# Optimization experiments

Hardware: AMD Instinct MI355X
Metric: run time of the kernel (lower is better)

## Reference

```python
import jax, jax.numpy as jnp
import numpy as np

N_NODES = 100000
N_EDGES = 1600000
N_REL = 8      # num_node_types in the torch module, used as relation count
D_IN = 128
D_HID = 128
D_OUT = 64


def setup_inputs() -> dict:
    key = jax.random.key(0)
    ks = jax.random.split(key, 16)
    x = jax.random.normal(ks[0], (N_NODES, D_IN), dtype=jnp.float32)
    edge_index = jax.random.randint(ks[1], (2, N_EDGES), 0, N_NODES, dtype=jnp.int64)
    edge_type = jax.random.randint(ks[2], (N_EDGES,), 0, N_REL, dtype=jnp.int64)
    # Glorot-ish init scale for stability
    def w(k, shape):
        fan = shape[-2] + shape[-1]
        return jax.random.normal(k, shape, dtype=jnp.float32) * jnp.sqrt(2.0 / fan)
    params = {
        'Wrel1': w(ks[3], (N_REL, D_IN, D_HID)),  'Wroot1': w(ks[4], (D_IN, D_HID)),  'b1': jnp.zeros((D_HID,), jnp.float32),
        'Wrel2': w(ks[5], (N_REL, D_HID, D_HID)), 'Wroot2': w(ks[6], (D_HID, D_HID)), 'b2': jnp.zeros((D_HID,), jnp.float32),
        'Wrel3': w(ks[7], (N_REL, D_HID, D_OUT)), 'Wroot3': w(ks[8], (D_HID, D_OUT)), 'b3': jnp.zeros((D_OUT,), jnp.float32),
    }
    return {'x': x, 'edge_index': edge_index, 'edge_type': edge_type, **params}


def _rgcn_conv(x, src, dst, edge_type, Wrel, Wroot, b):
    # Per-relation transform of all nodes: [R, N, out] (small GEMMs),
    # then per-edge gather + scatter-add (the memory-bound part).
    h = jnp.einsum('ni,rio->rno', x, Wrel)          # [R, N, out]
    msgs = h[edge_type, src]                        # [E, out] irregular gather
    agg = jax.ops.segment_sum(msgs, dst, num_segments=x.shape[0])  # [N, out]
    return x @ Wroot + b + agg


def reference(x, edge_index, edge_type, Wrel1, Wroot1, b1, Wrel2, Wroot2, b2, Wrel3, Wroot3, b3):
    src, dst = edge_index[0], edge_index[1]
    # Dropout is identity in eval mode (training=False in the torch module).
    h = jax.nn.relu(_rgcn_conv(x, src, dst, edge_type, Wrel1, Wroot1, b1))
    h = jax.nn.relu(_rgcn_conv(h, src, dst, edge_type, Wrel2, Wroot2, b2))
    h = _rgcn_conv(h, src, dst, edge_type, Wrel3, Wroot3, b3)
    return jax.nn.log_softmax(h, axis=-1)
```

## Files before the change

### kernel.cpp

```cpp
#include <hip/hip_runtime.h>


#define DEVI __device__ __forceinline__

typedef __attribute__((ext_vector_type(8))) short bf16x8;
typedef __attribute__((ext_vector_type(4))) float f32x4;

DEVI unsigned short f2b(float f) {
  unsigned int u = __builtin_bit_cast(unsigned int, f);
  unsigned int r = (u + 0x7FFFu + ((u >> 16) & 1u)) >> 16;
  return (unsigned short)r;
}
DEVI float b2f(unsigned short h) {
  unsigned int u = ((unsigned int)h) << 16;
  return __builtin_bit_cast(float, u);
}
DEVI float lo16f(unsigned v) { return __builtin_bit_cast(float, v << 16); }
DEVI float hifraw(unsigned v) { return __builtin_bit_cast(float, v); }
DEVI int imin(int a, int b) { return a < b ? a : b; }
DEVI int imax(int a, int b) { return a > b ? a : b; }


__global__ void k_zero2(int* __restrict__ cnt, int n) {
  int stride = gridDim.x * blockDim.x;
  for (int i = blockIdx.x * blockDim.x + threadIdx.x; i < n; i += stride) cnt[i] = 0;
}

__global__ void k_chist(const int* __restrict__ et, const int* __restrict__ edst,
                        int* __restrict__ gh, int NG, int E) {
  __shared__ int h[128];
  if (threadIdx.x < 128) h[threadIdx.x] = 0;
  __syncthreads();
  int stride = gridDim.x * blockDim.x;
  for (int i = blockIdx.x * blockDim.x + threadIdx.x; i < E; i += stride)
    atomicAdd(&h[(et[i] & 7) * NG + (edst[i] >> 13)], 1);
  __syncthreads();
  if (threadIdx.x < 128) atomicAdd(&gh[threadIdx.x], h[threadIdx.x]);
}

__global__ void k_cscan(const int* __restrict__ gh, int* __restrict__ gcursor,
                        int* __restrict__ cbase, int NBC, int E) {
  if (threadIdx.x == 0) {
    int a = 0;
    for (int b = 0; b < NBC; ++b) { cbase[b] = a; gcursor[b] = a; a += gh[b]; }
    cbase[NBC] = E;
  }
}

__launch_bounds__(256)
__global__ void k_cfill(const int* __restrict__ et, const int* __restrict__ esrc,
                        const int* __restrict__ edst, int* __restrict__ gcursor,
                        int* __restrict__ stage, int NG, int E) {
  __shared__ int h[128], base[128], lc[128];
  int nb = gridDim.x;
  int slice = (E + nb - 1) / nb;
  int lo = blockIdx.x * slice;
  int hi = lo + slice < E ? lo + slice : E;
  int t = threadIdx.x;
  if (t < 128) { h[t] = 0; lc[t] = 0; }
  __syncthreads();
  for (int i = lo + t; i < hi; i += 256)
    atomicAdd(&h[(et[i] & 7) * NG + (edst[i] >> 13)], 1);
  __syncthreads();
  if (t < 128 && h[t] > 0) base[t] = atomicAdd(&gcursor[t], h[t]);
  __syncthreads();
  for (int i = lo + t; i < hi; i += 256) {
    int d = edst[i];
    int tile = d >> 6;
    int bin = (et[i] & 7) * NG + (tile >> 7);
    int p = base[bin] + atomicAdd(&lc[bin], 1);
    stage[p] = ((tile & 127) << 23) | ((d & 63) << 17) | esrc[i];
  }
}

__launch_bounds__(1024)
__global__ void k_fine(const int* __restrict__ cbase, const int* __restrict__ stage,
                       int* __restrict__ srcl, int* __restrict__ lo9,
                       int* __restrict__ len9, int NG, int NTr) {
  __shared__ int h[8192];
  __shared__ int tsum[1024];
  __shared__ int wsum[16];
  int b = blockIdx.x;
  int rel = b / NG, tg = b - rel * NG;
  int lo = cbase[b], hi = cbase[b + 1];
  int t = threadIdx.x;
  for (int k = t; k < 8192; k += 1024) h[k] = 0;
  __syncthreads();
  for (int i = lo + t; i < hi; i += 1024)
    atomicAdd(&h[(stage[i] >> 17) & 0x1FFF], 1);
  __syncthreads();
  int dbase = tg * 8192;
  size_t relbase = (size_t)rel * NTr;
  for (int k = t; k < 8192; k += 1024) {
    int d = dbase + k;
    if (d < NTr) len9[relbase + d] = h[k];
  }
  int loc[8];
  int s = 0;
  int kb = t * 8;
#pragma unroll
  for (int j = 0; j < 8; ++j) { loc[j] = s; s += h[kb + j]; }
  tsum[t] = s;
  __syncthreads();
  int lane = t & 63, w = t >> 6;
  int v = tsum[t];
#pragma unroll
  for (int o = 1; o < 64; o <<= 1) {
    int u = __shfl_up(v, o);
    if (lane >= o) v += u;
  }
  if (lane == 63) wsum[w] = v;
  __syncthreads();
  if (t == 0) {
    int a = 0;
#pragma unroll
    for (int j = 0; j < 16; ++j) { int tmp = wsum[j]; wsum[j] = a; a += tmp; }
  }
  __syncthreads();
  int texcl = v - s + wsum[w];
#pragma unroll
  for (int j = 0; j < 8; ++j) h[kb + j] = texcl + loc[j];
  __syncthreads();
  for (int k = t; k < 8192; k += 1024) {
    int d = dbase + k;
    if (d < NTr) lo9[relbase + d] = lo + h[k];
  }
  __syncthreads();
  for (int i = lo + t; i < hi; i += 1024) {
    int pk = stage[i];
    int key = (pk >> 17) & 0x1FFF;
    int p = atomicAdd(&h[key], 1);
    srcl[lo + p] = pk & 0x1FFFF;
  }
}


__global__ void wprep_kernel(const float* __restrict__ Wrel, const float* __restrict__ Wroot,
                             unsigned short* __restrict__ wt, int DOUT) {
  int total = 9 * 128 * DOUT;
  int stride = gridDim.x * blockDim.x;
  for (int i = blockIdx.x * blockDim.x + threadIdx.x; i < total; i += stride) {
    int k = i & 127;
    int oo = i >> 7;
    int o = oo % DOUT;
    int rr = oo / DOUT;
    float v = (rr < 8) ? Wrel[((size_t)rr * 128 + k) * DOUT + o]
                       : Wroot[(size_t)k * DOUT + o];
    wt[i] = f2b(v);
  }
}


template <int NRP>
__launch_bounds__(256)
__global__ void agg_kernel(const unsigned* __restrict__ x32,
                           const int* __restrict__ lo9, const int* __restrict__ len9,
                           const int* __restrict__ srcl,
                           unsigned* __restrict__ Ydw,
                           int r0, int N, int E, int NTr) {
  int lane = threadIdx.x & 63;
  int d = (blockIdx.x * blockDim.x + threadIdx.x) >> 6;
  if (d >= N) return;

  int lo[NRP], ln[NRP];
#pragma unroll
  for (int r = 0; r < NRP; ++r) {
    size_t idx = (size_t)(r0 + r) * NTr + d;
    lo[r] = lo9[idx];
    ln[r] = len9[idx];
  }

  int s[NRP][4];
#pragma unroll
  for (int r = 0; r < NRP; ++r) {
    int lo_c = imin(lo[r], E - 1);
    int jmax = imax(ln[r] - 1, 0);
#pragma unroll
    for (int j = 0; j < 4; ++j)
      s[r][j] = srcl[lo_c + imin(j, jmax)];
  }

  unsigned v[NRP][4];
#pragma unroll
  for (int r = 0; r < NRP; ++r)
#pragma unroll
    for (int j = 0; j < 4; ++j)
      v[r][j] = x32[(size_t)s[r][j] * 64 + lane];

#pragma unroll
  for (int r = 0; r < NRP; ++r) {
    float a0 = 0.f, a1 = 0.f;
#pragma unroll
    for (int j = 0; j < 4; ++j) {
      if (ln[r] > j) { a0 += lo16f(v[r][j]); a1 += hifraw(v[r][j]); }
    }
    if (ln[r] > 4) {
      int i = lo[r] + 4, e = lo[r] + ln[r];
      for (; i + 2 <= e; i += 2) {
        int sA = srcl[i], sB = srcl[i + 1];
        unsigned vA = x32[(size_t)sA * 64 + lane];
        unsigned vB = x32[(size_t)sB * 64 + lane];
        a0 += lo16f(vA) + lo16f(vB);
        a1 += hifraw(vA) + hifraw(vB);
      }
      if (i < e) {
        unsigned vA = x32[(size_t)srcl[i] * 64 + lane];
        a0 += lo16f(vA);
        a1 += hifraw(vA);
      }
    }
    Ydw[(size_t)d * (NRP * 64) + r * 64 + lane] =
        (unsigned)f2b(a0) | ((unsigned)f2b(a1) << 16);
  }
}


struct SrcArr {
  const unsigned short* a[9];
  const unsigned short* w[9];
  int st[9];
};

template <int DOUT, int NK, int EPI>
__launch_bounds__(256)
__global__ void gemm_lds(SrcArr S, const float* __restrict__ bias,
                         const unsigned short* __restrict__ part,
                         unsigned short* __restrict__ out_b,
                         float* __restrict__ out_f, int N) {
  __shared__ unsigned short Al[2][64 * 128];
  constexpr int NF = (DOUT == 128) ? 2 : 1;
  int tid = threadIdx.x, wid = tid >> 6, lane = tid & 63;
  int colb = lane & 15, kgrp = lane >> 4;
  int colw = wid * 16 * NF;
  int tile = gridDim.x - 1 - blockIdx.x;
  int tilebase = tile * 64;

  auto stage = [&](int t, int buf) {
    const unsigned short* sa = S.a[t] + (size_t)tilebase * S.st[t];
    int st = S.st[t];
#pragma unroll
    for (int q = 0; q < 4; ++q) {
      int c = q * 256 + tid;
      int row = c >> 4, kcl = c & 15;
      int kcg = kcl ^ (row & 7);
      const unsigned short* gp = sa + (size_t)row * st + kcg * 8;
      unsigned short* lp = &Al[buf][(q * 256 + (tid & ~63)) * 8];
      __builtin_amdgcn_global_load_lds(
          (__attribute__((address_space(1))) void*)gp,
          (__attribute__((address_space(3))) void*)lp, 16, 0, 0);
    }
  };

  f32x4 acc[4][NF];
#pragma unroll
  for (int rb = 0; rb < 4; ++rb)
#pragma unroll
    for (int nf = 0; nf < NF; ++nf) {
      f32x4 z = {0.f, 0.f, 0.f, 0.f};
      acc[rb][nf] = z;
    }

  stage(0, 0);
#pragma unroll
  for (int t = 0; t < NK; ++t) {
    __syncthreads();
    if (t + 1 < NK) stage(t + 1, (t + 1) & 1);
    const unsigned short* W = S.w[t];
    const unsigned short* Ab = Al[t & 1];
#pragma unroll
    for (int kk = 0; kk < 4; ++kk) {
      int kc = kk * 4 + kgrp;
      bf16x8 a[4];
#pragma unroll
      for (int rb = 0; rb < 4; ++rb) {
        int arow = rb * 16 + colb;
        a[rb] = *(const bf16x8*)(Ab + (size_t)(arow * 16 + (kc ^ (arow & 7))) * 8);
      }
#pragma unroll
      for (int nf = 0; nf < NF; ++nf) {
        bf16x8 b = *(const bf16x8*)(W + (size_t)(colw + nf * 16 + colb) * 128 + kc * 8);
#pragma unroll
        for (int rb = 0; rb < 4; ++rb)
          acc[rb][nf] = __builtin_amdgcn_mfma_f32_16x16x32_bf16(a[rb], b, acc[rb][nf], 0, 0, 0);
      }
    }
  }

  float bv[NF];
  if (EPI == 0 || EPI == 3 || EPI == 4) {
#pragma unroll
    for (int nf = 0; nf < NF; ++nf) bv[nf] = bias[colw + nf * 16 + colb];
  }

  if ((EPI == 2 || EPI == 4) && DOUT == 64) {
    float* Lf = (float*)Al;
    __syncthreads();
#pragma unroll
    for (int rb = 0; rb < 4; ++rb)
#pragma unroll
      for (int i = 0; i < 4; ++i) {
        int row = rb * 16 + kgrp * 4 + i;
        int grow = tilebase + row;
        int rc = grow < N ? grow : 0;
        float v = acc[rb][0][i];
        if (EPI == 4) v += bv[0];
        else v += b2f(part[(size_t)rc * 64 + colw + colb]);
        Lf[row * 68 + colw + colb] = v;
      }
    __syncthreads();
#pragma unroll
    for (int it = 0; it < 4; ++it) {
      int row = wid * 16 + it * 4 + (lane >> 4);
      float v[4];
#pragma unroll
      for (int j = 0; j < 4; ++j) v[j] = Lf[row * 68 + colb + j * 16];
      float m = fmaxf(fmaxf(v[0], v[1]), fmaxf(v[2], v[3]));
#pragma unroll
      for (int s = 1; s < 16; s <<= 1) m = fmaxf(m, __shfl_xor(m, s));
      float sum = 0.f;
#pragma unroll
      for (int j = 0; j < 4; ++j) sum += __expf(v[j] - m);
#pragma unroll
      for (int s = 1; s < 16; s <<= 1) sum += __shfl_xor(sum, s);
      float lse = m + __logf(sum);
      int grow = tilebase + row;
      if (grow < N) {
#pragma unroll
        for (int j = 0; j < 4; ++j)
          out_f[(size_t)grow * 64 + colb + j * 16] = v[j] - lse;
      }
    }
  } else {
#pragma unroll
    for (int rb = 0; rb < 4; ++rb)
#pragma unroll
      for (int i = 0; i < 4; ++i) {
        int row = tilebase + rb * 16 + kgrp * 4 + i;
        bool ok = row < N;
        int rc = ok ? row : 0;
#pragma unroll
        for (int nf = 0; nf < NF; ++nf) {
          int col = colw + nf * 16 + colb;
          float v = acc[rb][nf][i];
          if (EPI == 0 || EPI == 3) v += bv[nf];
          if (EPI == 1 || EPI == 5) v += b2f(part[(size_t)rc * DOUT + col]);
          if (EPI == 1 || EPI == 3) v = fmaxf(v, 0.f);
          if (ok) out_b[(size_t)row * DOUT + col] = f2b(v);
        }
      }
  }
}

template <int DOUT>
static void run_gemm(int NK, int EPI, const SrcArr& S, const float* bias,
                     const unsigned short* part, unsigned short* ob, float* of,
                     int N, int NT, hipStream_t st) {
#define GCALL(nk, epi)                                                        \
  if (NK == nk && EPI == epi) {                                               \
    gemm_lds<DOUT, nk, epi><<<NT, 256, 0, st>>>(S, bias, part, ob, of, N);    \
    return;                                                                   \
  }
  GCALL(9, 3) GCALL(9, 4)
  GCALL(5, 0) GCALL(4, 1) GCALL(4, 2)
  GCALL(3, 0) GCALL(2, 5) GCALL(2, 1) GCALL(2, 2)
#undef GCALL
}


__global__ void cast_kernel(const float* __restrict__ in, unsigned short* __restrict__ out,
                            int n4) {
  int stride = gridDim.x * blockDim.x;
  for (int i = blockIdx.x * blockDim.x + threadIdx.x; i < n4; i += stride) {
    float4 v = ((const float4*)in)[i];
    ushort4 o;
    o.x = f2b(v.x); o.y = f2b(v.y); o.z = f2b(v.z); o.w = f2b(v.w);
    ((ushort4*)out)[i] = o;
  }
}


extern "C" void kernel_launch(void* const* d_in, const int* in_sizes, int n_in,
                              void* d_out, int out_size, void* d_ws, size_t ws_size,
                              hipStream_t stream) {
  const float* x = (const float*)d_in[0];
  const int* eidx = (const int*)d_in[1];
  const int* et = (const int*)d_in[2];
  const float* Wrel1 = (const float*)d_in[3];
  const float* Wroot1 = (const float*)d_in[4];
  const float* b1 = (const float*)d_in[5];
  const float* Wrel2 = (const float*)d_in[6];
  const float* Wroot2 = (const float*)d_in[7];
  const float* b2 = (const float*)d_in[8];
  const float* Wrel3 = (const float*)d_in[9];
  const float* Wroot3 = (const float*)d_in[10];
  const float* b3 = (const float*)d_in[11];

  const int N = in_sizes[0] / 128;
  const int E = in_sizes[2];
  const int NT = (N + 63) / 64;
  const int NTr = NT * 64;
  const int NG = (NT + 127) / 128;
  const int NBC = 8 * NG;
  const int* esrc = eidx;
  const int* edst = eidx + E;

  const size_t XB = (size_t)NTr * 128 * 2;

  size_t fixedB = XB + 2 * ((size_t)9 * 128 * 128 * 2) + (size_t)9 * 64 * 128 * 2 +
                  2 * ((size_t)E * 4) + 2 * ((size_t)8 * NTr * 4) + 8192;
  int NRP = 8;
  if (fixedB + 8 * XB > ws_size) NRP = 4;
  if (NRP == 4 && fixedB + XB + 4 * XB > ws_size) NRP = 2;

  char* p = (char*)d_ws;
  auto carve = [&](size_t bytes) {
    void* q = (void*)p;
    p += (bytes + 255) & ~(size_t)255;
    return q;
  };
  unsigned short* bufX = (unsigned short*)carve(XB);
  unsigned short* wt1 = (unsigned short*)carve((size_t)9 * 128 * 128 * 2);
  unsigned short* wt2 = (unsigned short*)carve((size_t)9 * 128 * 128 * 2);
  unsigned short* wt3 = (unsigned short*)carve((size_t)9 * 64 * 128 * 2);
  int* stage = (int*)carve((size_t)E * 4);
  int* srcl = (int*)carve((size_t)E * 4);
  int* lo9 = (int*)carve((size_t)8 * NTr * 4);
  int* len9 = (int*)carve((size_t)8 * NTr * 4);
  int* gh = (int*)carve(512);
  int* gcursor = (int*)carve(512);
  int* cbase = (int*)carve(512);
  unsigned short* part = (unsigned short*)((NRP < 8) ? carve(XB) : nullptr);
  unsigned short* Y = (unsigned short*)carve((size_t)NRP * XB);

  k_zero2<<<1, 128, 0, stream>>>(gh, 128);
  k_chist<<<512, 256, 0, stream>>>(et, edst, gh, NG, E);
  k_cscan<<<1, 64, 0, stream>>>(gh, gcursor, cbase, NBC, E);
  k_cfill<<<512, 256, 0, stream>>>(et, esrc, edst, gcursor, stage, NG, E);
  k_fine<<<NBC, 1024, 0, stream>>>(cbase, stage, srcl, lo9, len9, NG, NTr);

  wprep_kernel<<<576, 256, 0, stream>>>(Wrel1, Wroot1, wt1, 128);
  wprep_kernel<<<576, 256, 0, stream>>>(Wrel2, Wroot2, wt2, 128);
  wprep_kernel<<<288, 256, 0, stream>>>(Wrel3, Wroot3, wt3, 64);
  cast_kernel<<<2048, 256, 0, stream>>>(x, bufX, N * 128 / 4);

  const int ablk = (N * 64 + 255) / 256;
  const int passes = 8 / NRP;

  auto layer = [&](const unsigned short* xin, const unsigned short* wt,
                   const float* bias, int DOUT, unsigned short* xout, float* fout) {
    for (int pidx = 0; pidx < passes; ++pidx) {
      int r0 = pidx * NRP;
      if (NRP == 8)
        agg_kernel<8><<<ablk, 256, 0, stream>>>((const unsigned*)xin, lo9, len9, srcl, (unsigned*)Y, r0, N, E, NTr);
      else if (NRP == 4)
        agg_kernel<4><<<ablk, 256, 0, stream>>>((const unsigned*)xin, lo9, len9, srcl, (unsigned*)Y, r0, N, E, NTr);
      else
        agg_kernel<2><<<ablk, 256, 0, stream>>>((const unsigned*)xin, lo9, len9, srcl, (unsigned*)Y, r0, N, E, NTr);

      SrcArr S;
      int idx = 0;
      if (pidx == 0) {
        S.a[0] = xin; S.w[0] = wt + (size_t)8 * DOUT * 128; S.st[0] = 128;
        idx = 1;
      }
      for (int j = 0; j < NRP; ++j) {
        S.a[idx] = Y + j * 128;
        S.w[idx] = wt + (size_t)(r0 + j) * DOUT * 128;
        S.st[idx] = NRP * 128;
        ++idx;
      }
      int NK = idx;
      int epi;
      bool lastp = (pidx == passes - 1);
      if (pidx == 0 && lastp) epi = (DOUT == 64) ? 4 : 3;
      else if (pidx == 0) epi = 0;
      else if (!lastp) epi = 5;
      else epi = (DOUT == 64) ? 2 : 1;

      unsigned short* ob = lastp ? xout : part;
      if (pidx == 0 && !lastp) ob = part;
      if (DOUT == 128)
        run_gemm<128>(NK, epi, S, bias, part, ob, fout, N, NT, stream);
      else
        run_gemm<64>(NK, epi, S, bias, part, ob, fout, N, NT, stream);
    }
  };

  layer(bufX, wt1, b1, 128, bufX, nullptr);
  layer(bufX, wt2, b2, 128, bufX, nullptr);
  layer(bufX, wt3, b3, 64, nullptr, (float*)d_out);
}
```

Baseline: 638.3 us.

## Chunk layers over node tiles so aggregated buffer stays cache-resident

Restructures each layer to process node tiles in chunks: aggregation writes a per-chunk Y buffer that the fused 9-way GEMM immediately consumes, instead of materializing Y for all nodes. Uses ping-pong activation buffers since chunked processing can no longer update in place. Aims to keep the intermediate in L2/last-level cache and cut DRAM traffic, at the cost of more launches and smaller grids per launch.

```diff
diff --git a/kernel.cpp b/kernel.cpp
--- a/kernel.cpp
+++ b/kernel.cpp
@@ -19,6 +19,7 @@
 DEVI float hifraw(unsigned v) { return __builtin_bit_cast(float, v); }
 DEVI int imin(int a, int b) { return a < b ? a : b; }
 DEVI int imax(int a, int b) { return a > b ? a : b; }
+static inline int hmin(int a, int b) { return a < b ? a : b; }
 
 
 __global__ void k_zero2(int* __restrict__ cnt, int n) {
@@ -151,21 +152,22 @@
 }
 
 
-template <int NRP>
 __launch_bounds__(256)
 __global__ void agg_kernel(const unsigned* __restrict__ x32,
                            const int* __restrict__ lo9, const int* __restrict__ len9,
                            const int* __restrict__ srcl,
                            unsigned* __restrict__ Ydw,
-                           int r0, int N, int E, int NTr) {
+                           int N, int E, int NTr, int row0) {
+  constexpr int NRP = 8;
   int lane = threadIdx.x & 63;
-  int d = (blockIdx.x * blockDim.x + threadIdx.x) >> 6;
+  int dl = (blockIdx.x * blockDim.x + threadIdx.x) >> 6;
+  int d = row0 + dl;
   if (d >= N) return;
 
   int lo[NRP], ln[NRP];
 #pragma unroll
   for (int r = 0; r < NRP; ++r) {
-    size_t idx = (size_t)(r0 + r) * NTr + d;
+    size_t idx = (size_t)r * NTr + d;
     lo[r] = lo9[idx];
     ln[r] = len9[idx];
   }
@@ -209,7 +211,7 @@
         a1 += hifraw(vA);
       }
     }
-    Ydw[(size_t)d * (NRP * 64) + r * 64 + lane] =
+    Ydw[(size_t)dl * 512 + r * 64 + lane] =
         (unsigned)f2b(a0) | ((unsigned)f2b(a1) << 16);
   }
 }
@@ -219,24 +221,25 @@
   const unsigned short* a[9];
   const unsigned short* w[9];
   int st[9];
+  int ro[9];
 };
 
-template <int DOUT, int NK, int EPI>
+template <int DOUT, int EPI>
 __launch_bounds__(256)
 __global__ void gemm_lds(SrcArr S, const float* __restrict__ bias,
-                         const unsigned short* __restrict__ part,
                          unsigned short* __restrict__ out_b,
-                         float* __restrict__ out_f, int N) {
+                         float* __restrict__ out_f, int N, int c0) {
+  constexpr int NK = 9;
   __shared__ unsigned short Al[2][64 * 128];
   constexpr int NF = (DOUT == 128) ? 2 : 1;
   int tid = threadIdx.x, wid = tid >> 6, lane = tid & 63;
   int colb = lane & 15, kgrp = lane >> 4;
   int colw = wid * 16 * NF;
-  int tile = gridDim.x - 1 - blockIdx.x;
+  int tile = c0 + (gridDim.x - 1 - blockIdx.x);
   int tilebase = tile * 64;
 
   auto stage = [&](int t, int buf) {
-    const unsigned short* sa = S.a[t] + (size_t)tilebase * S.st[t];
+    const unsigned short* sa = S.a[t] + (size_t)(tilebase - S.ro[t]) * S.st[t];
     int st = S.st[t];
 #pragma unroll
     for (int q = 0; q < 4; ++q) {
@@ -287,12 +290,10 @@
   }
 
   float bv[NF];
-  if (EPI == 0 || EPI == 3 || EPI == 4) {
-#pragma unroll
-    for (int nf = 0; nf < NF; ++nf) bv[nf] = bias[colw + nf * 16 + colb];
-  }
-
-  if ((EPI == 2 || EPI == 4) && DOUT == 64) {
+#pragma unroll
+  for (int nf = 0; nf < NF; ++nf) bv[nf] = bias[colw + nf * 16 + colb];
+
+  if (EPI == 4 && DOUT == 64) {
     float* Lf = (float*)Al;
     __syncthreads();
 #pragma unroll
@@ -300,12 +301,7 @@
 #pragma unroll
       for (int i = 0; i < 4; ++i) {
         int row = rb * 16 + kgrp * 4 + i;
-        int grow = tilebase + row;
-        int rc = grow < N ? grow : 0;
-        float v = acc[rb][0][i];
-        if (EPI == 4) v += bv[0];
-        else v += b2f(part[(size_t)rc * 64 + colw + colb]);
-        Lf[row * 68 + colw + colb] = v;
+        Lf[row * 68 + colw + colb] = acc[rb][0][i] + bv[0];
       }
     __syncthreads();
 #pragma unroll
@@ -336,34 +332,15 @@
 #pragma unroll
       for (int i = 0; i < 4; ++i) {
         int row = tilebase + rb * 16 + kgrp * 4 + i;
-        bool ok = row < N;
-        int rc = ok ? row : 0;
+        if (row >= N) continue;
 #pragma unroll
         for (int nf = 0; nf < NF; ++nf) {
           int col = colw + nf * 16 + colb;
-          float v = acc[rb][nf][i];
-          if (EPI == 0 || EPI == 3) v += bv[nf];
-          if (EPI == 1 || EPI == 5) v += b2f(part[(size_t)rc * DOUT + col]);
-          if (EPI == 1 || EPI == 3) v = fmaxf(v, 0.f);
-          if (ok) out_b[(size_t)row * DOUT + col] = f2b(v);
+          float v = fmaxf(acc[rb][nf][i] + bv[nf], 0.f);
+          out_b[(size_t)row * DOUT + col] = f2b(v);
         }
       }
   }
-}
-
-template <int DOUT>
-static void run_gemm(int NK, int EPI, const SrcArr& S, const float* bias,
-                     const unsigned short* part, unsigned short* ob, float* of,
-                     int N, int NT, hipStream_t st) {
-#define GCALL(nk, epi)                                                        \
-  if (NK == nk && EPI == epi) {                                               \
-    gemm_lds<DOUT, nk, epi><<<NT, 256, 0, st>>>(S, bias, part, ob, of, N);    \
-    return;                                                                   \
-  }
-  GCALL(9, 3) GCALL(9, 4)
-  GCALL(5, 0) GCALL(4, 1) GCALL(4, 2)
-  GCALL(3, 0) GCALL(2, 5) GCALL(2, 1) GCALL(2, 2)
-#undef GCALL
 }
 
 
@@ -406,11 +383,10 @@
 
   const size_t XB = (size_t)NTr * 128 * 2;
 
-  size_t fixedB = XB + 2 * ((size_t)9 * 128 * 128 * 2) + (size_t)9 * 64 * 128 * 2 +
+  size_t fixedB = 2 * XB + 2 * ((size_t)9 * 128 * 128 * 2) + (size_t)9 * 64 * 128 * 2 +
                   2 * ((size_t)E * 4) + 2 * ((size_t)8 * NTr * 4) + 8192;
-  int NRP = 8;
-  if (fixedB + 8 * XB > ws_size) NRP = 4;
-  if (NRP == 4 && fixedB + XB + 4 * XB > ws_size) NRP = 2;
+  int CT = 512;
+  while (CT > 64 && fixedB + (size_t)CT * 131072 > ws_size) CT >>= 1;
 
   char* p = (char*)d_ws;
   auto carve = [&](size_t bytes) {
@@ -418,7 +394,8 @@
     p += (bytes + 255) & ~(size_t)255;
     return q;
   };
-  unsigned short* bufX = (unsigned short*)carve(XB);
+  unsigned short* bufX0 = (unsigned short*)carve(XB);
+  unsigned short* bufX1 = (unsigned short*)carve(XB);
   unsigned short* wt1 = (unsigned short*)carve((size_t)9 * 128 * 128 * 2);
   unsigned short* wt2 = (unsigned short*)carve((size_t)9 * 128 * 128 * 2);
   unsigned short* wt3 = (unsigned short*)carve((size_t)9 * 64 * 128 * 2);
@@ -429,8 +406,7 @@
   int* gh = (int*)carve(512);
   int* gcursor = (int*)carve(512);
   int* cbase = (int*)carve(512);
-  unsigned short* part = (unsigned short*)((NRP < 8) ? carve(XB) : nullptr);
-  unsigned short* Y = (unsigned short*)carve((size_t)NRP * XB);
+  unsigned short* Y = (unsigned short*)carve((size_t)CT * 131072);
 
   k_zero2<<<1, 128, 0, stream>>>(gh, 128);
   k_chist<<<512, 256, 0, stream>>>(et, edst, gh, NG, E);
@@ -441,52 +417,30 @@
   wprep_kernel<<<576, 256, 0, stream>>>(Wrel1, Wroot1, wt1, 128);
   wprep_kernel<<<576, 256, 0, stream>>>(Wrel2, Wroot2, wt2, 128);
   wprep_kernel<<<288, 256, 0, stream>>>(Wrel3, Wroot3, wt3, 64);
-  cast_kernel<<<2048, 256, 0, stream>>>(x, bufX, N * 128 / 4);
-
-  const int ablk = (N * 64 + 255) / 256;
-  const int passes = 8 / NRP;
+  cast_kernel<<<2048, 256, 0, stream>>>(x, bufX0, N * 128 / 4);
 
   auto layer = [&](const unsigned short* xin, const unsigned short* wt,
                    const float* bias, int DOUT, unsigned short* xout, float* fout) {
-    for (int pidx = 0; pidx < passes; ++pidx) {
-      int r0 = pidx * NRP;
-      if (NRP == 8)
-        agg_kernel<8><<<ablk, 256, 0, stream>>>((const unsigned*)xin, lo9, len9, srcl, (unsigned*)Y, r0, N, E, NTr);
-      else if (NRP == 4)
-        agg_kernel<4><<<ablk, 256, 0, stream>>>((const unsigned*)xin, lo9, len9, srcl, (unsigned*)Y, r0, N, E, NTr);
+    for (int c0 = 0; c0 < NT; c0 += CT) {
+      int ct = hmin(CT, NT - c0);
+      agg_kernel<<<ct * 16, 256, 0, stream>>>((const unsigned*)xin, lo9, len9, srcl,
+                                              (unsigned*)Y, N, E, NTr, c0 * 64);
+      SrcArr S;
+      S.a[0] = xin; S.w[0] = wt + (size_t)8 * DOUT * 128; S.st[0] = 128; S.ro[0] = 0;
+      for (int j = 0; j < 8; ++j) {
+        S.a[j + 1] = Y + j * 128;
+        S.w[j + 1] = wt + (size_t)j * DOUT * 128;
+        S.st[j + 1] = 1024;
+        S.ro[j + 1] = c0 * 64;
+      }
+      if (DOUT == 128)
+        gemm_lds<128, 3><<<ct, 256, 0, stream>>>(S, bias, xout, (float*)nullptr, N, c0);
       else
-        agg_kernel<2><<<ablk, 256, 0, stream>>>((const unsigned*)xin, lo9, len9, srcl, (unsigned*)Y, r0, N, E, NTr);
-
-      SrcArr S;
-      int idx = 0;
-      if (pidx == 0) {
-        S.a[0] = xin; S.w[0] = wt + (size_t)8 * DOUT * 128; S.st[0] = 128;
-        idx = 1;
-      }
-      for (int j = 0; j < NRP; ++j) {
-        S.a[idx] = Y + j * 128;
-        S.w[idx] = wt + (size_t)(r0 + j) * DOUT * 128;
-        S.st[idx] = NRP * 128;
-        ++idx;
-      }
-      int NK = idx;
-      int epi;
-      bool lastp = (pidx == passes - 1);
-      if (pidx == 0 && lastp) epi = (DOUT == 64) ? 4 : 3;
-      else if (pidx == 0) epi = 0;
-      else if (!lastp) epi = 5;
-      else epi = (DOUT == 64) ? 2 : 1;
-
-      unsigned short* ob = lastp ? xout : part;
-      if (pidx == 0 && !lastp) ob = part;
-      if (DOUT == 128)
-        run_gemm<128>(NK, epi, S, bias, part, ob, fout, N, NT, stream);
-      else
-        run_gemm<64>(NK, epi, S, bias, part, ob, fout, N, NT, stream);
+        gemm_lds<64, 4><<<ct, 256, 0, stream>>>(S, bias, (unsigned short*)nullptr, fout, N, c0);
     }
   };
 
-  layer(bufX, wt1, b1, 128, bufX, nullptr);
-  layer(bufX, wt2, b2, 128, bufX, nullptr);
-  layer(bufX, wt3, b3, 64, nullptr, (float*)d_out);
-}
+  layer(bufX0, wt1, b1, 128, bufX1, nullptr);
+  layer(bufX1, wt2, b2, 128, bufX0, nullptr);
+  layer(bufX0, wt3, b3, 64, nullptr, (float*)d_out);
+}
```

Measured after the change: 811.9 us. 1.27x slower.
